# Performance work log

Hardware: AMD Instinct MI355X
Metric: run time of the kernel (lower is better)

## Reference

```python
import jax, jax.numpy as jnp
import numpy as np

B, C_IN, H, W = 32, 3, 224, 224
D_MODEL, DEPTH = 192, 24
D_INNER, D_STATE, DT_RANK, D_CONV = 384, 16, 12, 4
PATCH = 16
NPATCH = (H // PATCH) * (W // PATCH)   # 196
TOKEN_POS = NPATCH // 2                # middle cls token position (98)
L = NPATCH + 1                         # 197 tokens
NUM_CLASSES = 1000
EPS = 1e-5


def setup_inputs() -> dict:
    key = jax.random.key(0)
    ks = iter(jax.random.split(key, 48))
    def nrm(shape, s=0.02):
        return jax.random.normal(next(ks), shape, jnp.float32) * s
    d = {}
    d["x"] = jax.random.normal(next(ks), (B, C_IN, H, W), jnp.float32)
    d["patch_w"] = nrm((D_MODEL, C_IN, PATCH, PATCH), 0.05)
    d["patch_b"] = jnp.zeros((D_MODEL,), jnp.float32)
    d["cls_token"] = nrm((1, 1, D_MODEL))
    d["pos_embed"] = nrm((1, L, D_MODEL))
    d["norm_w"] = jnp.ones((DEPTH, D_MODEL), jnp.float32)
    d["in_proj_w"] = nrm((DEPTH, 2 * D_INNER, D_MODEL))
    # Mamba S4D-real init: A_log[d,n] = log(n+1)
    A0 = jnp.broadcast_to(jnp.log(jnp.arange(1, D_STATE + 1, dtype=jnp.float32)), (DEPTH, D_INNER, D_STATE))
    for sfx in ("", "_b"):
        d["conv_w" + sfx] = nrm((DEPTH, D_INNER, D_CONV), 0.2)
        d["conv_b" + sfx] = jnp.zeros((DEPTH, D_INNER), jnp.float32)
        d["xproj_w" + sfx] = nrm((DEPTH, DT_RANK + 2 * D_STATE, D_INNER))
        d["dtproj_w" + sfx] = nrm((DEPTH, D_INNER, DT_RANK), 0.1)
        d["dtproj_b" + sfx] = jnp.full((DEPTH, D_INNER), -4.0, jnp.float32)  # softplus(-4) ~ small dt init
        d["A_log" + sfx] = A0
        d["D" + sfx] = jnp.ones((DEPTH, D_INNER), jnp.float32)
    d["out_proj_w"] = nrm((DEPTH, D_MODEL, D_INNER))
    d["normf_w"] = jnp.ones((D_MODEL,), jnp.float32)
    d["head_w"] = nrm((NUM_CLASSES, D_MODEL))
    d["head_b"] = jnp.zeros((NUM_CLASSES,), jnp.float32)
    return d


def _rms(x, w):
    return x * jax.lax.rsqrt(jnp.mean(x * x, -1, keepdims=True) + EPS) * w


def _causal_conv_silu(x, w, b):
    # x: [B,L,Din]; w: [Din,K] depthwise causal conv (conv1d padded left, truncated to L)
    Lx = x.shape[1]
    xp = jnp.pad(x, ((0, 0), (D_CONV - 1, 0), (0, 0)))
    y = sum(w[:, k] * xp[:, k:k + Lx] for k in range(D_CONV)) + b
    return jax.nn.silu(y)


def _ssm(x, dt, Bs, Cs, A, Dp):
    # selective scan: h_t = exp(dt_t*A)*h_{t-1} + dt_t*B_t*x_t ; y_t = <h_t, C_t> + D*x_t
    def step(h, inp):
        xt, dtt, Bt, Ct = inp  # [B,Din],[B,Din],[B,N],[B,N]
        h = jnp.exp(dtt[..., None] * A) * h + (dtt * xt)[..., None] * Bt[:, None, :]
        return h, jnp.einsum('bdn,bn->bd', h, Ct)
    h0 = jnp.zeros((x.shape[0], D_INNER, D_STATE), x.dtype)
    xs = tuple(jnp.moveaxis(t, 1, 0) for t in (x, dt, Bs, Cs))
    _, ys = jax.lax.scan(step, h0, xs)
    return jnp.moveaxis(ys, 0, 1) + x * Dp


def _mamba_dir(xz, conv_w, conv_b, xproj_w, dtproj_w, dtproj_b, A_log, Dp):
    x, z = jnp.split(xz, 2, axis=-1)
    x = _causal_conv_silu(x, conv_w, conv_b)
    dbc = jnp.einsum('bld,ed->ble', x, xproj_w)
    dt = jax.nn.softplus(jnp.einsum('blr,dr->bld', dbc[..., :DT_RANK], dtproj_w) + dtproj_b)
    Bs = dbc[..., DT_RANK:DT_RANK + D_STATE]
    Cs = dbc[..., DT_RANK + D_STATE:]
    y = _ssm(x, dt, Bs, Cs, -jnp.exp(A_log), Dp)
    return y * jax.nn.silu(z)


def _block(carry, p):
    hidden, residual = carry
    residual = residual + hidden          # fused add-norm: add then norm (prenorm)
    hs = _rms(residual, p["norm_w"])
    xz = jnp.einsum('bld,ed->ble', hs, p["in_proj_w"])
    yf = _mamba_dir(xz, p["conv_w"], p["conv_b"], p["xproj_w"], p["dtproj_w"], p["dtproj_b"], p["A_log"], p["D"])
    yb = _mamba_dir(xz[:, ::-1], p["conv_w_b"], p["conv_b_b"], p["xproj_w_b"], p["dtproj_w_b"], p["dtproj_b_b"], p["A_log_b"], p["D_b"])[:, ::-1]
    out = jnp.einsum('ble,de->bld', (yf + yb) * 0.5, p["out_proj_w"])  # if_divide_out
    return (out, residual), None


def _forward(x, patch_w, patch_b, cls_token, pos_embed, norm_w, in_proj_w,
             conv_w, conv_b, xproj_w, dtproj_w, dtproj_b, A_log, D,
             conv_w_b, conv_b_b, xproj_w_b, dtproj_w_b, dtproj_b_b, A_log_b, D_b,
             out_proj_w, normf_w, head_w, head_b):
    # patch embed: 16x16 stride-16 conv -> [B, 196, 192]
    feat = jax.lax.conv_general_dilated(x, patch_w, (PATCH, PATCH), 'VALID',
                                        dimension_numbers=('NCHW', 'OIHW', 'NCHW'))
    feat = (feat + patch_b[None, :, None, None]).reshape(x.shape[0], D_MODEL, NPATCH).transpose(0, 2, 1)
    tok = jnp.broadcast_to(cls_token, (x.shape[0], 1, D_MODEL))
    h = jnp.concatenate([feat[:, :TOKEN_POS], tok, feat[:, TOKEN_POS:]], axis=1) + pos_embed
    lp = dict(norm_w=norm_w, in_proj_w=in_proj_w, conv_w=conv_w, conv_b=conv_b,
              xproj_w=xproj_w, dtproj_w=dtproj_w, dtproj_b=dtproj_b, A_log=A_log, D=D,
              conv_w_b=conv_w_b, conv_b_b=conv_b_b, xproj_w_b=xproj_w_b, dtproj_w_b=dtproj_w_b,
              dtproj_b_b=dtproj_b_b, A_log_b=A_log_b, D_b=D_b, out_proj_w=out_proj_w)
    (hidden, residual), _ = jax.lax.scan(jax.checkpoint(_block), (h, jnp.zeros_like(h)), lp)
    y = _rms(hidden + residual, normf_w)
    return y[:, TOKEN_POS] @ head_w.T + head_b  # [B, num_classes]


def reference(x, patch_w, patch_b, cls_token, pos_embed, norm_w, in_proj_w,
              conv_w, conv_b, xproj_w, dtproj_w, dtproj_b, A_log, D,
              conv_w_b, conv_b_b, xproj_w_b, dtproj_w_b, dtproj_b_b, A_log_b, D_b,
              out_proj_w, normf_w, head_w, head_b):
    return _forward(x, patch_w, patch_b, cls_token, pos_embed, norm_w, in_proj_w,
                    conv_w, conv_b, xproj_w, dtproj_w, dtproj_b, A_log, D,
                    conv_w_b, conv_b_b, xproj_w_b, dtproj_w_b, dtproj_b_b, A_log_b, D_b,
                    out_proj_w, normf_w, head_w, head_b)
```

## Files before the change

kernel.cpp:

```cpp
#include <hip/hip_runtime.h>
#include <math.h>

#define NB 32
#define SL 197
#define DM 192
#define DI 384
#define NS 16
#define NLAYER 24
#define NCLS 1000
#define TOKPOS 98
#define EPSF 1e-5f
#define NTOK (NB * SL)
#define NTOKP 6336
#define YSTRIDE 6528
#define CH 32

#define PL_IW 147456
#define PL_OW 73728
#define PL_XP 33792
#define PL_SET (2*PL_IW + 2*PL_OW + 2*PL_XP)

struct DirW { const float *cw, *cb, *xpw, *dtw, *dtb; };

typedef __attribute__((ext_vector_type(8))) short short8v;
typedef __attribute__((ext_vector_type(4))) float f32x4;

__device__ __forceinline__ float siluf(float x) { return x / (1.f + __expf(-x)); }
__device__ __forceinline__ float softplusf(float x) {
  return (x > 20.f) ? x : log1pf(__expf(x));
}
__device__ __forceinline__ ushort f2bf(float v) {
  uint u = __float_as_uint(v);
  u += 0x7FFF + ((u >> 16) & 1);
  return (ushort)(u >> 16);
}
__device__ __forceinline__ float bf2f(ushort h) { return __uint_as_float(((uint)h) << 16); }

__global__ __launch_bounds__(256) void k_wsplit0(
    const float* __restrict__ pw, const float* __restrict__ cls,
    const float* __restrict__ pos, ushort* __restrict__ pwh,
    ushort* __restrict__ pwl, float* __restrict__ res) {
  int i = blockIdx.x * 256 + threadIdx.x;
  float v = pw[i];
  ushort h = f2bf(v);
  pwh[i] = h; pwl[i] = f2bf(v - bf2f(h));
  if (i < NB * DM) {
    int b = i / DM, col = i % DM;
    res[(size_t)(b * SL + TOKPOS) * DM + col] = cls[col] + pos[TOKPOS * DM + col];
  }
}

__global__ __launch_bounds__(256) void k_wsplit(
    const float* __restrict__ win, const float* __restrict__ wout,
    const float* __restrict__ xpwf, const float* __restrict__ xpwb,
    ushort* __restrict__ planes) {
  int L = blockIdx.y;
  const float* w1 = win  + (size_t)L * PL_IW;
  const float* w2 = wout + (size_t)L * PL_OW;
  const float* w3 = xpwf + (size_t)L * (PL_XP / 2);
  const float* w4 = xpwb + (size_t)L * (PL_XP / 2);
  ushort* s = planes + (size_t)L * PL_SET;
  ushort* iwh = s;
  ushort* iwl = s + PL_IW;
  ushort* owh = s + 2 * PL_IW;
  ushort* owl = s + 2 * PL_IW + PL_OW;
  ushort* xph = s + 2 * PL_IW + 2 * PL_OW;
  ushort* xpl = s + 2 * PL_IW + 2 * PL_OW + PL_XP;
  int i = blockIdx.x * 256 + threadIdx.x;
  {
    float v = w1[i];
    ushort h = f2bf(v);
    iwh[i] = h; iwl[i] = f2bf(v - bf2f(h));
  }
  if (i < PL_OW) {
    float v = w2[i];
    ushort h = f2bf(v);
    owh[i] = h; owl[i] = f2bf(v - bf2f(h));
  }
  if (i < PL_XP / 2) {
    float v = w3[i];
    ushort h = f2bf(v);
    xph[i] = h; xpl[i] = f2bf(v - bf2f(h));
    v = w4[i];
    h = f2bf(v);
    xph[PL_XP / 2 + i] = h; xpl[PL_XP / 2 + i] = f2bf(v - bf2f(h));
  }
}

__global__ __launch_bounds__(256) void k_patch(
    const float* __restrict__ x, const ushort* __restrict__ pwh,
    const ushort* __restrict__ pwl, const float* __restrict__ pb,
    const float* __restrict__ pos, float* __restrict__ res) {
  __shared__ __align__(16) ushort Ahi[32][40], Alo[32][40];
  __shared__ __align__(16) ushort Whi[192][40], Wlo[192][40];
  int tid = threadIdx.x;
  int m0 = blockIdx.x * 32;
  int kk = tid & 31;
  size_t xoff[4];
#pragma unroll
  for (int it = 0; it < 4; ++it) {
    int t = (tid >> 5) + it * 8;
    int gp = m0 + t, b = gp / 196, p = gp % 196;
    int ph = p / 14, pwi = p % 14;
    xoff[it] = (size_t)(b * 3) * 50176 + (size_t)(ph * 16) * 224 + pwi * 16;
  }
  int lane = tid & 63, wid = tid >> 6;
  int wm = wid >> 1, wn = wid & 1;
  int lr = lane & 15, ls = lane >> 4;
  f32x4 acc[6];
#pragma unroll
  for (int nf = 0; nf < 6; ++nf) acc[nf] = f32x4{0.f, 0.f, 0.f, 0.f};

  for (int c = 0; c < 24; ++c) {
    __syncthreads();
#pragma unroll
    for (int it = 0; it < 4; ++it) {
      int t = (tid >> 5) + it * 8;
      int k = c * 32 + kk;
      int ch = k >> 8, r = (k >> 4) & 15, cc = k & 15;
      float v = x[xoff[it] + (size_t)ch * 50176 + r * 224 + cc];
      ushort h = f2bf(v);
      Ahi[t][kk] = h; Alo[t][kk] = f2bf(v - bf2f(h));
    }
#pragma unroll
    for (int it = 0; it < 12; ++it) {
      int i = tid + it * 256;
      int r = i >> 4, kp = i & 15;
      size_t ui = (size_t)r * 384 + c * 16 + kp;
      uint vh = ((const uint*)pwh)[ui];
      uint vl = ((const uint*)pwl)[ui];
      *(uint*)&Whi[r][kp * 2] = vh;
      *(uint*)&Wlo[r][kp * 2] = vl;
    }
    __syncthreads();
    short8v ah = *(const short8v*)&Ahi[wm * 16 + lr][ls * 8];
    short8v al = *(const short8v*)&Alo[wm * 16 + lr][ls * 8];
#pragma unroll
    for (int nf = 0; nf < 6; ++nf) {
      short8v bh = *(const short8v*)&Whi[wn * 96 + nf * 16 + lr][ls * 8];
      short8v bl = *(const short8v*)&Wlo[wn * 96 + nf * 16 + lr][ls * 8];
      acc[nf] = __builtin_amdgcn_mfma_f32_16x16x32_bf16(ah, bh, acc[nf], 0, 0, 0);
      acc[nf] = __builtin_amdgcn_mfma_f32_16x16x32_bf16(ah, bl, acc[nf], 0, 0, 0);
      acc[nf] = __builtin_amdgcn_mfma_f32_16x16x32_bf16(al, bh, acc[nf], 0, 0, 0);
    }
  }
  {
    int tokp = m0 + wm * 16 + ls * 4;
#pragma unroll
    for (int nf = 0; nf < 6; ++nf) {
      int col = wn * 96 + nf * 16 + lr;
      f32x4 a = acc[nf];
#pragma unroll
      for (int rr = 0; rr < 4; ++rr) {
        int gp = tokp + rr, b = gp / 196, p = gp % 196;
        int l = p + (p >= TOKPOS);
        res[(size_t)(b * SL + l) * DM + col] = a[rr] + pb[col] + pos[l * DM + col];
      }
    }
  }
}

__global__ __launch_bounds__(256) void k_rms_inproj(
    const float* __restrict__ res, const float* __restrict__ nw,
    const ushort* __restrict__ iwh, const ushort* __restrict__ iwl,
    float* __restrict__ xz) {
  __shared__ __align__(16) ushort Ahi[64][40], Alo[64][40];
  __shared__ __align__(16) ushort Whi[192][40], Wlo[192][40];
  __shared__ float scl[64];
  int tid = threadIdx.x;
  int m0 = blockIdx.x * 64, n0 = blockIdx.y * 192;
  {
    int tok = tid >> 2, q = tid & 3;
    const float* rp = res + (size_t)(m0 + tok) * 192 + q;
    float s = 0.f;
#pragma unroll
    for (int j = 0; j < 48; ++j) { float v = rp[4 * j]; s += v * v; }
    s += __shfl_xor(s, 1, 4); s += __shfl_xor(s, 2, 4);
    if (q == 0) scl[tok] = rsqrtf(s * (1.f / 192.f) + EPSF);
  }
  __syncthreads();

  int lane = tid & 63, wid = tid >> 6;
  int wm = wid >> 1, wn = wid & 1;
  int lr = lane & 15, ls = lane >> 4;
  f32x4 acc[2][6];
#pragma unroll
  for (int mf = 0; mf < 2; ++mf)
#pragma unroll
    for (int nf = 0; nf < 6; ++nf) acc[mf][nf] = f32x4{0.f, 0.f, 0.f, 0.f};

  for (int c = 0; c < 6; ++c) {
    int k0 = c * 32;
    __syncthreads();
#pragma unroll
    for (int it = 0; it < 8; ++it) {
      int i = tid + it * 256;
      int t = i >> 5, kk = i & 31;
      float v = res[(size_t)(m0 + t) * 192 + k0 + kk] * scl[t] * nw[k0 + kk];
      ushort h = f2bf(v);
      Ahi[t][kk] = h; Alo[t][kk] = f2bf(v - bf2f(h));
    }
#pragma unroll
    for (int it = 0; it < 12; ++it) {
      int i = tid + it * 256;
      int r = i >> 4, kp = i & 15;
      size_t ui = (size_t)(n0 + r) * 96 + (k0 >> 1) + kp;
      uint vh = ((const uint*)iwh)[ui];
      uint vl = ((const uint*)iwl)[ui];
      *(uint*)&Whi[r][kp * 2] = vh;
      *(uint*)&Wlo[r][kp * 2] = vl;
    }
    __syncthreads();
    short8v ah0 = *(const short8v*)&Ahi[wm * 32 + lr][ls * 8];
    short8v ah1 = *(const short8v*)&Ahi[wm * 32 + 16 + lr][ls * 8];
    short8v al0 = *(const short8v*)&Alo[wm * 32 + lr][ls * 8];
    short8v al1 = *(const short8v*)&Alo[wm * 32 + 16 + lr][ls * 8];
#pragma unroll
    for (int nf = 0; nf < 6; ++nf) {
      short8v bh = *(const short8v*)&Whi[wn * 96 + nf * 16 + lr][ls * 8];
      short8v bl = *(const short8v*)&Wlo[wn * 96 + nf * 16 + lr][ls * 8];
      acc[0][nf] = __builtin_amdgcn_mfma_f32_16x16x32_bf16(ah0, bh, acc[0][nf], 0, 0, 0);
      acc[1][nf] = __builtin_amdgcn_mfma_f32_16x16x32_bf16(ah1, bh, acc[1][nf], 0, 0, 0);
      acc[0][nf] = __builtin_amdgcn_mfma_f32_16x16x32_bf16(ah0, bl, acc[0][nf], 0, 0, 0);
      acc[1][nf] = __builtin_amdgcn_mfma_f32_16x16x32_bf16(ah1, bl, acc[1][nf], 0, 0, 0);
      acc[0][nf] = __builtin_amdgcn_mfma_f32_16x16x32_bf16(al0, bh, acc[0][nf], 0, 0, 0);
      acc[1][nf] = __builtin_amdgcn_mfma_f32_16x16x32_bf16(al1, bh, acc[1][nf], 0, 0, 0);
    }
  }
#pragma unroll
  for (int mf = 0; mf < 2; ++mf) {
    int tok = m0 + wm * 32 + mf * 16 + ls * 4;
#pragma unroll
    for (int nf = 0; nf < 6; ++nf) {
      int col = n0 + wn * 96 + nf * 16 + lr;
      f32x4 a = acc[mf][nf];
      xz[(size_t)(tok + 0) * 768 + col] = a[0];
      xz[(size_t)(tok + 1) * 768 + col] = a[1];
      xz[(size_t)(tok + 2) * 768 + col] = a[2];
      xz[(size_t)(tok + 3) * 768 + col] = a[3];
    }
  }
}

__global__ __launch_bounds__(256) void k_proj(
    const float* __restrict__ xz, DirW wf, DirW wb,
    const ushort* __restrict__ xpwh, const ushort* __restrict__ xpwl,
    float* __restrict__ xc, float* __restrict__ dt,
    float* __restrict__ Bs, float* __restrict__ Cs) {
  __shared__ __align__(16) ushort Ahi[16][104], Alo[16][104];
  __shared__ __align__(16) ushort Whi[48][104], Wlo[48][104];
  __shared__ __align__(16) float dbc[16][64];
  int g = blockIdx.x;
  int dir = blockIdx.y;
  int tid = threadIdx.x;
  DirW w = dir ? wb : wf;
  const ushort* wh = xpwh + (size_t)dir * (PL_XP / 2);
  const ushort* wl = xpwl + (size_t)dir * (PL_XP / 2);
  int base = dir * NTOK;
  int m0 = g * 16;

  int dd = tid & 31;
  int t0 = tid >> 5;
  int mr0 = m0 + t0, mr1 = m0 + t0 + 8;
  int bb0 = mr0 / SL, lr0 = mr0 % SL;
  int bb1 = mr1 / SL, lr1 = mr1 % SL;

  int lane = tid & 63, wn = tid >> 6;
  int lr = lane & 15, ls = lane >> 4;
  f32x4 acc = f32x4{0.f, 0.f, 0.f, 0.f};

  for (int c = 0; c < 4; ++c) {
    __syncthreads();
#pragma unroll
    for (int kg = 0; kg < 3; ++kg) {
      int k0 = c * 96 + kg * 32;
      int d = k0 + dd;
      float cw0 = w.cw[d * 4 + 0], cw1 = w.cw[d * 4 + 1];
      float cw2 = w.cw[d * 4 + 2], cw3 = w.cw[d * 4 + 3];
      float cb = w.cb[d];
#pragma unroll
      for (int half = 0; half < 2; ++half) {
        int t = half ? (t0 + 8) : t0;
        int bb = half ? bb1 : bb0, lrr = half ? lr1 : lr0;
        float a = cb;
        {
          int p = lrr - 3;
          if (p >= 0) a += cw0 * xz[(size_t)(bb * SL + (dir ? SL - 1 - p : p)) * 768 + d];
          p = lrr - 2;
          if (p >= 0) a += cw1 * xz[(size_t)(bb * SL + (dir ? SL - 1 - p : p)) * 768 + d];
          p = lrr - 1;
          if (p >= 0) a += cw2 * xz[(size_t)(bb * SL + (dir ? SL - 1 - p : p)) * 768 + d];
          p = lrr;
          a += cw3 * xz[(size_t)(bb * SL + (dir ? SL - 1 - p : p)) * 768 + d];
        }
        float v = siluf(a);
        xc[(size_t)(base + m0 + t) * DI + d] = v;
        ushort h = f2bf(v);
        Ahi[t][kg * 32 + dd] = h; Alo[t][kg * 32 + dd] = f2bf(v - bf2f(h));
      }
    }
#pragma unroll
    for (int it = 0; it < 9; ++it) {
      int i = tid + it * 256;
      int r = i / 48, kp = i % 48;
      uint vh = 0, vl = 0;
      if (r < 44) {
        size_t ui = (size_t)r * 192 + c * 48 + kp;
        vh = ((const uint*)wh)[ui];
        vl = ((const uint*)wl)[ui];
      }
      *(uint*)&Whi[r][kp * 2] = vh;
      *(uint*)&Wlo[r][kp * 2] = vl;
    }
    __syncthreads();
    if (wn < 3) {
#pragma unroll
      for (int ks = 0; ks < 3; ++ks) {
        short8v ah = *(const short8v*)&Ahi[lr][ls * 8 + ks * 32];
        short8v al = *(const short8v*)&Alo[lr][ls * 8 + ks * 32];
        short8v bh = *(const short8v*)&Whi[wn * 16 + lr][ls * 8 + ks * 32];
        short8v bl = *(const short8v*)&Wlo[wn * 16 + lr][ls * 8 + ks * 32];
        acc = __builtin_amdgcn_mfma_f32_16x16x32_bf16(ah, bh, acc, 0, 0, 0);
        acc = __builtin_amdgcn_mfma_f32_16x16x32_bf16(ah, bl, acc, 0, 0, 0);
        acc = __builtin_amdgcn_mfma_f32_16x16x32_bf16(al, bh, acc, 0, 0, 0);
      }
    }
  }
  __syncthreads();
  if (wn < 3) {
#pragma unroll
    for (int r = 0; r < 4; ++r)
      dbc[ls * 4 + r][wn * 16 + lr] = acc[r];
  }
  __syncthreads();

#pragma unroll
  for (int it = 0; it < 2; ++it) {
    int i = tid + it * 256;
    int t = i >> 5, e = i & 31;
    float v = dbc[t][12 + e];
    int mr = m0 + t;
    if (e < 16) Bs[(size_t)(base + mr) * NS + e] = v;
    else        Cs[(size_t)(base + mr) * NS + (e - 16)] = v;
  }

#pragma unroll
  for (int pass = 0; pass < 2; ++pass) {
    int d = tid + pass * 256;
    if (d < 384) {
      float wr_[12];
#pragma unroll
      for (int r = 0; r < 12; ++r) wr_[r] = w.dtw[d * 12 + r];
      float bias = w.dtb[d];
      for (int t = 0; t < 16; ++t) {
        float4 q0 = *reinterpret_cast<const float4*>(&dbc[t][0]);
        float4 q1 = *reinterpret_cast<const float4*>(&dbc[t][4]);
        float4 q2 = *reinterpret_cast<const float4*>(&dbc[t][8]);
        float s = bias
          + q0.x * wr_[0] + q0.y * wr_[1] + q0.z * wr_[2] + q0.w * wr_[3]
          + q1.x * wr_[4] + q1.y * wr_[5] + q1.z * wr_[6] + q1.w * wr_[7]
          + q2.x * wr_[8] + q2.y * wr_[9] + q2.z * wr_[10] + q2.w * wr_[11];
        dt[(size_t)(base + m0 + t) * DI + d] = softplusf(s);
      }
    }
  }
}

__global__ __launch_bounds__(128) void k_scan(
    const float* __restrict__ xc, const float* __restrict__ dt,
    const float* __restrict__ Bs, const float* __restrict__ Cs,
    const float* __restrict__ Alog0, const float* __restrict__ Alog1,
    const float* __restrict__ D0, const float* __restrict__ D1,
    float* __restrict__ y) {
  __shared__ float2 sdtx[2][CH][32];
  __shared__ float sB[2][CH][16], sC[2][CH][16];
  int tid = threadIdx.x;
  int dloc = tid >> 2, nq = tid & 3;
  int d0 = blockIdx.x * 32;
  int b = blockIdx.y, dir = blockIdx.z;
  int d = d0 + dloc;
  const float* Alog = dir ? Alog1 : Alog0;
  float a2[4], h[4];
#pragma unroll
  for (int j = 0; j < 4; ++j) {
    a2[j] = -__expf(Alog[d * NS + nq * 4 + j]) * 1.44269504088896340736f;
    h[j] = 0.f;
  }
  float Dp = (dir ? D1 : D0)[d];
  int base = dir * NTOK + b * SL;
  const float* dtp = dt + (size_t)base * DI + d0;
  const float* xp  = xc + (size_t)base * DI + d0;
  const float* Bp  = Bs + (size_t)base * NS;
  const float* Cp  = Cs + (size_t)base * NS;
  float* yp = y + ((size_t)dir * YSTRIDE + (size_t)b * SL) * DI + d;

#pragma unroll
  for (int k = 0; k < 8; ++k) {
    int idx = tid + k * 128;
    int l = idx >> 5, ddx = idx & 31;
    sdtx[0][l][ddx] = make_float2(dtp[l * DI + ddx], xp[l * DI + ddx]);
  }
#pragma unroll
  for (int k = 0; k < 4; ++k) {
    int idx = tid + k * 128;
    int l = idx >> 4, j = idx & 15;
    sB[0][l][j] = Bp[l * NS + j];
    sC[0][l][j] = Cp[l * NS + j];
  }
  __syncthreads();

  const int nch = (SL + CH - 1) / CH;
  for (int c = 0; c < nch; ++c) {
    int cur = c & 1;
    float pd[8], px[8], pB[4], pC[4];
    if (c + 1 < nch) {
      int l0n = (c + 1) * CH;
#pragma unroll
      for (int k = 0; k < 8; ++k) {
        int idx = tid + k * 128;
        int l = l0n + (idx >> 5), ddx = idx & 31;
        bool gq = l < SL;
        pd[k] = gq ? dtp[l * DI + ddx] : 0.f;
        px[k] = gq ? xp[l * DI + ddx] : 0.f;
      }
#pragma unroll
      for (int k = 0; k < 4; ++k) {
        int idx = tid + k * 128;
        int l = l0n + (idx >> 4), j = idx & 15;
        bool gq = l < SL;
        pB[k] = gq ? Bp[l * NS + j] : 0.f;
        pC[k] = gq ? Cp[l * NS + j] : 0.f;
      }
    }
    int l0 = c * CH;
    int steps = min(CH, SL - l0);
    for (int s = 0; s < steps; ++s) {
      float2 dx = sdtx[cur][s][dloc];
      float4 Bv = *reinterpret_cast<const float4*>(&sB[cur][s][nq * 4]);
      float4 Cv = *reinterpret_cast<const float4*>(&sC[cur][s][nq * 4]);
      float ps = dx.x * dx.y;
      float yv;
      h[0] = exp2f(a2[0] * dx.x) * h[0] + ps * Bv.x; yv  = h[0] * Cv.x;
      h[1] = exp2f(a2[1] * dx.x) * h[1] + ps * Bv.y; yv += h[1] * Cv.y;
      h[2] = exp2f(a2[2] * dx.x) * h[2] + ps * Bv.z; yv += h[2] * Cv.z;
      h[3] = exp2f(a2[3] * dx.x) * h[3] + ps * Bv.w; yv += h[3] * Cv.w;
      yv += __shfl_xor(yv, 1, 4);
      yv += __shfl_xor(yv, 2, 4);
      if (nq == 0) yp[(l0 + s) * DI] = yv + dx.y * Dp;
    }
    if (c + 1 < nch) {
#pragma unroll
      for (int k = 0; k < 8; ++k) {
        int idx = tid + k * 128;
        int l = idx >> 5, ddx = idx & 31;
        sdtx[cur ^ 1][l][ddx] = make_float2(pd[k], px[k]);
      }
#pragma unroll
      for (int k = 0; k < 4; ++k) {
        int idx = tid + k * 128;
        int l = idx >> 4, j = idx & 15;
        sB[cur ^ 1][l][j] = pB[k];
        sC[cur ^ 1][l][j] = pC[k];
      }
    }
    __syncthreads();
  }
}

__global__ __launch_bounds__(256) void k_gate_outproj(
    const float* __restrict__ y, const float* __restrict__ xz,
    const ushort* __restrict__ owh, const ushort* __restrict__ owl,
    float* __restrict__ res) {
  __shared__ __align__(16) ushort Ahi[64][40], Alo[64][40];
  __shared__ __align__(16) ushort Whi[192][40], Wlo[192][40];
  int tid = threadIdx.x;
  int m0 = blockIdx.x * 64;
  int ks = blockIdx.y;
  int lane = tid & 63, wid = tid >> 6;
  int wm = wid >> 1, wn = wid & 1;
  int lr = lane & 15, ls = lane >> 4;
  f32x4 acc[2][6];
#pragma unroll
  for (int mf = 0; mf < 2; ++mf)
#pragma unroll
    for (int nf = 0; nf < 6; ++nf) acc[mf][nf] = f32x4{0.f, 0.f, 0.f, 0.f};

  for (int c = 0; c < 6; ++c) {
    int k0 = ks * 192 + c * 32;
    __syncthreads();
#pragma unroll
    for (int it = 0; it < 8; ++it) {
      int i = tid + it * 256;
      int t = i >> 5, kk = i & 31;
      int m = m0 + t;
      int b = m / SL, p = m % SL;
      float yf  = y[(size_t)(b * SL + p) * 384 + k0 + kk];
      float ybk = y[((size_t)YSTRIDE + b * SL + (SL - 1 - p)) * 384 + k0 + kk];
      float z = xz[(size_t)m * 768 + 384 + k0 + kk];
      float v = 0.5f * (yf + ybk) * siluf(z);
      ushort h = f2bf(v);
      Ahi[t][kk] = h; Alo[t][kk] = f2bf(v - bf2f(h));
    }
#pragma unroll
    for (int it = 0; it < 12; ++it) {
      int i = tid + it * 256;
      int r = i >> 4, kp = i & 15;
      size_t ui = (size_t)r * 192 + (k0 >> 1) + kp;
      uint vh = ((const uint*)owh)[ui];
      uint vl = ((const uint*)owl)[ui];
      *(uint*)&Whi[r][kp * 2] = vh;
      *(uint*)&Wlo[r][kp * 2] = vl;
    }
    __syncthreads();
    short8v ah0 = *(const short8v*)&Ahi[wm * 32 + lr][ls * 8];
    short8v ah1 = *(const short8v*)&Ahi[wm * 32 + 16 + lr][ls * 8];
    short8v al0 = *(const short8v*)&Alo[wm * 32 + lr][ls * 8];
    short8v al1 = *(const short8v*)&Alo[wm * 32 + 16 + lr][ls * 8];
#pragma unroll
    for (int nf = 0; nf < 6; ++nf) {
      short8v bh = *(const short8v*)&Whi[wn * 96 + nf * 16 + lr][ls * 8];
      short8v bl = *(const short8v*)&Wlo[wn * 96 + nf * 16 + lr][ls * 8];
      acc[0][nf] = __builtin_amdgcn_mfma_f32_16x16x32_bf16(ah0, bh, acc[0][nf], 0, 0, 0);
      acc[1][nf] = __builtin_amdgcn_mfma_f32_16x16x32_bf16(ah1, bh, acc[1][nf], 0, 0, 0);
      acc[0][nf] = __builtin_amdgcn_mfma_f32_16x16x32_bf16(ah0, bl, acc[0][nf], 0, 0, 0);
      acc[1][nf] = __builtin_amdgcn_mfma_f32_16x16x32_bf16(ah1, bl, acc[1][nf], 0, 0, 0);
      acc[0][nf] = __builtin_amdgcn_mfma_f32_16x16x32_bf16(al0, bh, acc[0][nf], 0, 0, 0);
      acc[1][nf] = __builtin_amdgcn_mfma_f32_16x16x32_bf16(al1, bh, acc[1][nf], 0, 0, 0);
    }
  }
#pragma unroll
  for (int mf = 0; mf < 2; ++mf) {
    int tok = m0 + wm * 32 + mf * 16 + ls * 4;
#pragma unroll
    for (int nf = 0; nf < 6; ++nf) {
      int col = wn * 96 + nf * 16 + lr;
      f32x4 a = acc[mf][nf];
      atomicAdd(&res[(size_t)(tok + 0) * 192 + col], a[0]);
      atomicAdd(&res[(size_t)(tok + 1) * 192 + col], a[1]);
      atomicAdd(&res[(size_t)(tok + 2) * 192 + col], a[2]);
      atomicAdd(&res[(size_t)(tok + 3) * 192 + col], a[3]);
    }
  }
}

__global__ __launch_bounds__(256) void k_head(
    const float* __restrict__ res, const float* __restrict__ nfw,
    const float* __restrict__ hw, const float* __restrict__ hb,
    float* __restrict__ out) {
  __shared__ float v[192];
  __shared__ float red[4];
  int b = blockIdx.x, tid = threadIdx.x;
  int m = b * SL + TOKPOS;
  float val = 0.f;
  if (tid < 192) val = res[(size_t)m * 192 + tid];
  float s = val * val;
#pragma unroll
  for (int o = 32; o; o >>= 1) s += __shfl_down(s, o, 64);
  if ((tid & 63) == 0) red[tid >> 6] = s;
  __syncthreads();
  if (tid == 0) {
    float t = red[0] + red[1] + red[2] + red[3];
    red[0] = rsqrtf(t * (1.f / 192.f) + EPSF);
  }
  __syncthreads();
  if (tid < 192) v[tid] = val * red[0] * nfw[tid];
  __syncthreads();
  for (int c = tid; c < NCLS; c += 256) {
    const float* wr = hw + c * 192;
    float acc = hb[c];
    for (int d = 0; d < 192; d += 4) {
      float4 w = *reinterpret_cast<const float4*>(wr + d);
      acc += w.x * v[d] + w.y * v[d + 1] + w.z * v[d + 2] + w.w * v[d + 3];
    }
    out[b * NCLS + c] = acc;
  }
}

extern "C" void kernel_launch(void* const* d_in, const int* in_sizes, int n_in,
                              void* d_out, int out_size, void* d_ws, size_t ws_size,
                              hipStream_t stream) {
  const float* x       = (const float*)d_in[0];
  const float* patch_w = (const float*)d_in[1];
  const float* patch_b = (const float*)d_in[2];
  const float* cls_tk  = (const float*)d_in[3];
  const float* pos_e   = (const float*)d_in[4];
  const float* norm_w  = (const float*)d_in[5];
  const float* in_w    = (const float*)d_in[6];
  const float* conv_w  = (const float*)d_in[7];
  const float* conv_b  = (const float*)d_in[8];
  const float* xproj_w = (const float*)d_in[9];
  const float* dtw     = (const float*)d_in[10];
  const float* dtb     = (const float*)d_in[11];
  const float* A_log   = (const float*)d_in[12];
  const float* Dvec    = (const float*)d_in[13];
  const float* conv_wb = (const float*)d_in[14];
  const float* conv_bb = (const float*)d_in[15];
  const float* xproj_wb= (const float*)d_in[16];
  const float* dtwb    = (const float*)d_in[17];
  const float* dtbb    = (const float*)d_in[18];
  const float* A_logb  = (const float*)d_in[19];
  const float* Dvecb   = (const float*)d_in[20];
  const float* out_w   = (const float*)d_in[21];
  const float* normf_w = (const float*)d_in[22];
  const float* head_w  = (const float*)d_in[23];
  const float* head_b  = (const float*)d_in[24];

  float* ws  = (float*)d_ws;
  float* res = ws;
  float* xz  = res + (size_t)NTOKP * DM;
  float* xc  = xz + (size_t)NTOKP * 768;
  float* dtB = xc + 2 * (size_t)NTOK * DI;
  float* Bsb = dtB + 2 * (size_t)NTOK * DI;
  float* Csb = Bsb + 2 * (size_t)NTOK * NS;
  float* yb  = Csb + 2 * (size_t)NTOK * NS;
  ushort* pwh = (ushort*)(yb + 2 * (size_t)YSTRIDE * DI);
  ushort* pwl = pwh + 147456;
  ushort* planes = pwl + 147456;

  size_t need24 = (size_t)((char*)(planes + (size_t)24 * PL_SET) - (char*)d_ws);
  bool pre = ws_size >= need24;

  k_wsplit0<<<dim3(576), dim3(256), 0, stream>>>(patch_w, cls_tk, pos_e, pwh, pwl, res);
  if (pre)
    k_wsplit<<<dim3(576, 24), dim3(256), 0, stream>>>(in_w, out_w, xproj_w, xproj_wb, planes);

  k_patch<<<dim3(196), dim3(256), 0, stream>>>(x, pwh, pwl, patch_b, pos_e, res);

  for (int layer = 0; layer < NLAYER; ++layer) {
    ushort* s = planes + (pre ? (size_t)layer * PL_SET : 0);
    if (!pre)
      k_wsplit<<<dim3(576, 1), dim3(256), 0, stream>>>(
          in_w + (size_t)layer * PL_IW, out_w + (size_t)layer * PL_OW,
          xproj_w + (size_t)layer * (PL_XP / 2), xproj_wb + (size_t)layer * (PL_XP / 2), s);
    ushort* iwh = s;
    ushort* iwl = s + PL_IW;
    ushort* owh = s + 2 * PL_IW;
    ushort* owl = s + 2 * PL_IW + PL_OW;
    ushort* xph = s + 2 * PL_IW + 2 * PL_OW;
    ushort* xpl = s + 2 * PL_IW + 2 * PL_OW + PL_XP;

    k_rms_inproj<<<dim3(NTOKP / 64, 4), dim3(256), 0, stream>>>(
        res, norm_w + layer * DM, iwh, iwl, xz);

    DirW wfd { conv_w  + layer * DI * 4, conv_b  + layer * DI,
               xproj_w + layer * 44 * DI, dtw  + layer * DI * 12, dtb  + layer * DI };
    DirW wbd { conv_wb + layer * DI * 4, conv_bb + layer * DI,
               xproj_wb+ layer * 44 * DI, dtwb + layer * DI * 12, dtbb + layer * DI };
    k_proj<<<dim3(NTOK / 16, 2), dim3(256), 0, stream>>>(
        xz, wfd, wbd, xph, xpl, xc, dtB, Bsb, Csb);

    k_scan<<<dim3(DI / 32, NB, 2), dim3(128), 0, stream>>>(
        xc, dtB, Bsb, Csb,
        A_log + (size_t)layer * DI * NS, A_logb + (size_t)layer * DI * NS,
        Dvec + layer * DI, Dvecb + layer * DI, yb);

    k_gate_outproj<<<dim3(NTOKP / 64, 2), dim3(256), 0, stream>>>(
        yb, xz, owh, owl, res);
  }

  k_head<<<dim3(NB), dim3(256), 0, stream>>>(res, normf_w, head_w, head_b, (float*)d_out);
}
```

Measured before the change: 4.897 ms.

## Retile gate/out_proj to 16-token blocks without split-K atomics; unroll scan

The gate+out_proj kernel changes from 64-token tiles with a two-way split over K to 16-token tiles that each cover the full K of 384. Each output element is then written once with a plain read-modify-write instead of atomicAdd. The cost is re-loading the full weight slice for every 16-token block, which adds weight traffic through LDS. Separately, the scan inner loop is fully unrolled over the chunk, with a bounds guard on the store, and the exp2 terms are computed before the FMA updates to expose more ILP.

```diff
diff --git a/kernel.cpp b/kernel.cpp
--- a/kernel.cpp
+++ b/kernel.cpp
@@ -433,20 +433,24 @@
       }
     }
     int l0 = c * CH;
-    int steps = min(CH, SL - l0);
-    for (int s = 0; s < steps; ++s) {
+#pragma unroll
+    for (int s = 0; s < CH; ++s) {
       float2 dx = sdtx[cur][s][dloc];
       float4 Bv = *reinterpret_cast<const float4*>(&sB[cur][s][nq * 4]);
       float4 Cv = *reinterpret_cast<const float4*>(&sC[cur][s][nq * 4]);
+      float e0 = exp2f(a2[0] * dx.x);
+      float e1 = exp2f(a2[1] * dx.x);
+      float e2 = exp2f(a2[2] * dx.x);
+      float e3 = exp2f(a2[3] * dx.x);
       float ps = dx.x * dx.y;
-      float yv;
-      h[0] = exp2f(a2[0] * dx.x) * h[0] + ps * Bv.x; yv  = h[0] * Cv.x;
-      h[1] = exp2f(a2[1] * dx.x) * h[1] + ps * Bv.y; yv += h[1] * Cv.y;
-      h[2] = exp2f(a2[2] * dx.x) * h[2] + ps * Bv.z; yv += h[2] * Cv.z;
-      h[3] = exp2f(a2[3] * dx.x) * h[3] + ps * Bv.w; yv += h[3] * Cv.w;
+      h[0] = fmaf(e0, h[0], ps * Bv.x);
+      h[1] = fmaf(e1, h[1], ps * Bv.y);
+      h[2] = fmaf(e2, h[2], ps * Bv.z);
+      h[3] = fmaf(e3, h[3], ps * Bv.w);
+      float yv = h[0] * Cv.x + h[1] * Cv.y + h[2] * Cv.z + h[3] * Cv.w;
       yv += __shfl_xor(yv, 1, 4);
       yv += __shfl_xor(yv, 2, 4);
-      if (nq == 0) yp[(l0 + s) * DI] = yv + dx.y * Dp;
+      if (nq == 0 && (l0 + s < SL)) yp[(l0 + s) * DI] = fmaf(dx.y, Dp, yv);
     }
     if (c + 1 < nch) {
 #pragma unroll
@@ -471,25 +475,21 @@
     const float* __restrict__ y, const float* __restrict__ xz,
     const ushort* __restrict__ owh, const ushort* __restrict__ owl,
     float* __restrict__ res) {
-  __shared__ __align__(16) ushort Ahi[64][40], Alo[64][40];
+  __shared__ __align__(16) ushort Ahi[16][40], Alo[16][40];
   __shared__ __align__(16) ushort Whi[192][40], Wlo[192][40];
   int tid = threadIdx.x;
-  int m0 = blockIdx.x * 64;
-  int ks = blockIdx.y;
-  int lane = tid & 63, wid = tid >> 6;
-  int wm = wid >> 1, wn = wid & 1;
+  int m0 = blockIdx.x * 16;
+  int lane = tid & 63, wn = tid >> 6;
   int lr = lane & 15, ls = lane >> 4;
-  f32x4 acc[2][6];
-#pragma unroll
-  for (int mf = 0; mf < 2; ++mf)
-#pragma unroll
-    for (int nf = 0; nf < 6; ++nf) acc[mf][nf] = f32x4{0.f, 0.f, 0.f, 0.f};
-
-  for (int c = 0; c < 6; ++c) {
-    int k0 = ks * 192 + c * 32;
-    __syncthreads();
-#pragma unroll
-    for (int it = 0; it < 8; ++it) {
+  f32x4 acc[3];
+#pragma unroll
+  for (int nf = 0; nf < 3; ++nf) acc[nf] = f32x4{0.f, 0.f, 0.f, 0.f};
+
+  for (int c = 0; c < 12; ++c) {
+    int k0 = c * 32;
+    __syncthreads();
+#pragma unroll
+    for (int it = 0; it < 2; ++it) {
       int i = tid + it * 256;
       int t = i >> 5, kk = i & 31;
       int m = m0 + t;
@@ -512,33 +512,25 @@
       *(uint*)&Wlo[r][kp * 2] = vl;
     }
     __syncthreads();
-    short8v ah0 = *(const short8v*)&Ahi[wm * 32 + lr][ls * 8];
-    short8v ah1 = *(const short8v*)&Ahi[wm * 32 + 16 + lr][ls * 8];
-    short8v al0 = *(const short8v*)&Alo[wm * 32 + lr][ls * 8];
-    short8v al1 = *(const short8v*)&Alo[wm * 32 + 16 + lr][ls * 8];
-#pragma unroll
-    for (int nf = 0; nf < 6; ++nf) {
-      short8v bh = *(const short8v*)&Whi[wn * 96 + nf * 16 + lr][ls * 8];
-      short8v bl = *(const short8v*)&Wlo[wn * 96 + nf * 16 + lr][ls * 8];
-      acc[0][nf] = __builtin_amdgcn_mfma_f32_16x16x32_bf16(ah0, bh, acc[0][nf], 0, 0, 0);
-      acc[1][nf] = __builtin_amdgcn_mfma_f32_16x16x32_bf16(ah1, bh, acc[1][nf], 0, 0, 0);
-      acc[0][nf] = __builtin_amdgcn_mfma_f32_16x16x32_bf16(ah0, bl, acc[0][nf], 0, 0, 0);
-      acc[1][nf] = __builtin_amdgcn_mfma_f32_16x16x32_bf16(ah1, bl, acc[1][nf], 0, 0, 0);
-      acc[0][nf] = __builtin_amdgcn_mfma_f32_16x16x32_bf16(al0, bh, acc[0][nf], 0, 0, 0);
-      acc[1][nf] = __builtin_amdgcn_mfma_f32_16x16x32_bf16(al1, bh, acc[1][nf], 0, 0, 0);
-    }
-  }
-#pragma unroll
-  for (int mf = 0; mf < 2; ++mf) {
-    int tok = m0 + wm * 32 + mf * 16 + ls * 4;
-#pragma unroll
-    for (int nf = 0; nf < 6; ++nf) {
-      int col = wn * 96 + nf * 16 + lr;
-      f32x4 a = acc[mf][nf];
-      atomicAdd(&res[(size_t)(tok + 0) * 192 + col], a[0]);
-      atomicAdd(&res[(size_t)(tok + 1) * 192 + col], a[1]);
-      atomicAdd(&res[(size_t)(tok + 2) * 192 + col], a[2]);
-      atomicAdd(&res[(size_t)(tok + 3) * 192 + col], a[3]);
+    short8v ah = *(const short8v*)&Ahi[lr][ls * 8];
+    short8v al = *(const short8v*)&Alo[lr][ls * 8];
+#pragma unroll
+    for (int nf = 0; nf < 3; ++nf) {
+      short8v bh = *(const short8v*)&Whi[wn * 48 + nf * 16 + lr][ls * 8];
+      short8v bl = *(const short8v*)&Wlo[wn * 48 + nf * 16 + lr][ls * 8];
+      acc[nf] = __builtin_amdgcn_mfma_f32_16x16x32_bf16(ah, bh, acc[nf], 0, 0, 0);
+      acc[nf] = __builtin_amdgcn_mfma_f32_16x16x32_bf16(ah, bl, acc[nf], 0, 0, 0);
+      acc[nf] = __builtin_amdgcn_mfma_f32_16x16x32_bf16(al, bh, acc[nf], 0, 0, 0);
+    }
+  }
+#pragma unroll
+  for (int nf = 0; nf < 3; ++nf) {
+    int col = wn * 48 + nf * 16 + lr;
+    f32x4 a = acc[nf];
+#pragma unroll
+    for (int rr = 0; rr < 4; ++rr) {
+      int tok = m0 + ls * 4 + rr;
+      res[(size_t)tok * 192 + col] += a[rr];
     }
   }
 }
@@ -654,7 +646,7 @@
         A_log + (size_t)layer * DI * NS, A_logb + (size_t)layer * DI * NS,
         Dvec + layer * DI, Dvecb + layer * DI, yb);
 
-    k_gate_outproj<<<dim3(NTOKP / 64, 2), dim3(256), 0, stream>>>(
+    k_gate_outproj<<<dim3(NTOKP / 16), dim3(256), 0, stream>>>(
         yb, xz, owh, owl, res);
   }
 
```

Result: faster. 4.247 ms (-13.3%).
